# Kernel optimization log

Measured on AMD Instinct MI355X. Metric: run time of the kernel, lower is better.

Reference implementation:

```python
import jax, jax.numpy as jnp
import numpy as np

NB_HEAD = 16
DIM_PER_HEAD = 64
EMB = 1024
B, SQ, SK = 4, 2048, 2048


def setup_inputs() -> dict:
    key = jax.random.key(0)
    ks = jax.random.split(key, 8)
    scale = 1.0 / np.sqrt(EMB)
    return {
        "hidden_state_query": jax.random.normal(ks[0], (B, SQ, EMB), jnp.float32),
        "hidden_state_key": jax.random.normal(ks[1], (B, SK, EMB), jnp.float32),
        "hidden_state_value": jax.random.normal(ks[2], (B, SK, EMB), jnp.float32),
        "attention_mask": jax.random.randint(ks[3], (B, SQ, SK), 0, 2).astype(bool),
        "Wq": jax.random.uniform(ks[4], (NB_HEAD * DIM_PER_HEAD, EMB), jnp.float32, -scale, scale),
        "Wk": jax.random.uniform(ks[5], (NB_HEAD * DIM_PER_HEAD, EMB), jnp.float32, -scale, scale),
        "Wv": jax.random.uniform(ks[6], (NB_HEAD * DIM_PER_HEAD, EMB), jnp.float32, -scale, scale),
        "Wo": jax.random.uniform(ks[7], (EMB, NB_HEAD * DIM_PER_HEAD), jnp.float32, -scale, scale),
    }


def reference(hidden_state_query, hidden_state_key, hidden_state_value,
              attention_mask, Wq, Wk, Wv, Wo):
    bs, sq, _ = hidden_state_query.shape
    sk = hidden_state_key.shape[1]
    # projections (nn.Linear without bias: x @ W.T)
    q = (hidden_state_query @ Wq.T).reshape(bs, sq, NB_HEAD, DIM_PER_HEAD).transpose(0, 2, 1, 3)
    k = (hidden_state_key @ Wk.T).reshape(bs, sk, NB_HEAD, DIM_PER_HEAD).transpose(0, 2, 1, 3)
    v = (hidden_state_value @ Wv.T).reshape(bs, sk, NB_HEAD, DIM_PER_HEAD).transpose(0, 2, 1, 3)
    scores = jnp.einsum('bhqd,bhkd->bhqk', q, k) / jnp.sqrt(jnp.asarray(DIM_PER_HEAD, q.dtype))
    attn = jax.nn.softmax(scores, axis=-1)
    # POST-softmax zero masking (True -> 0), broadcast over heads; no renormalization
    attn = jnp.where(attention_mask[:, None, :, :], jnp.asarray(0.0, attn.dtype), attn)
    ctx = jnp.einsum('bhqk,bhkd->bhqd', attn, v)  # [B,H,Sq,Dh]
    ctx = ctx.transpose(0, 2, 1, 3).reshape(bs, sq, NB_HEAD * DIM_PER_HEAD)
    return ctx @ Wo.T + hidden_state_query
```

## Files before the change

kernel.cpp:

```cpp
#include <hip/hip_runtime.h>
#include <hip/hip_bf16.h>
#include <stdint.h>

typedef __bf16 bf16_t;
typedef bf16_t bf16x2 __attribute__((ext_vector_type(2)));
typedef bf16_t bf16x8 __attribute__((ext_vector_type(8)));
typedef float  f32x4  __attribute__((ext_vector_type(4)));
typedef float  f32x16 __attribute__((ext_vector_type(16)));
typedef unsigned uint2v __attribute__((ext_vector_type(2)));

#define NB_HEAD 16
#define DH      64
#define EMB     1024
#define BATCH   4
#define SEQ     2048
#define NTOK    (BATCH*SEQ)

#define QSCALE 0.1803368801111204f

__device__ __forceinline__ void gload_lds16(const void* g, void* l) {
  __builtin_amdgcn_global_load_lds(
      (const __attribute__((address_space(1))) void*)g,
      (__attribute__((address_space(3))) void*)l, 16, 0, 0);
}

__device__ __forceinline__ uint32_t pkbf(float a, float b) {
  bf16x2 v = { (bf16_t)a, (bf16_t)b };
  return __builtin_bit_cast(uint32_t, v);
}

__device__ __forceinline__ void cvt8_body(const float* __restrict__ in,
                                          bf16_t* __restrict__ out, int i) {
  const float4* p = reinterpret_cast<const float4*>(in) + (size_t)i * 2;
  float4 a = p[0], b = p[1];
  uint4 r;
  r.x = pkbf(a.x, a.y); r.y = pkbf(a.z, a.w);
  r.z = pkbf(b.x, b.y); r.w = pkbf(b.z, b.w);
  reinterpret_cast<uint4*>(out)[i] = r;
}

__device__ __forceinline__ void mkand_body(const uint8_t* __restrict__ m,
                                           uint16_t* __restrict__ out, int i) {
  uint2 v = reinterpret_cast<const uint2*>(m)[i];
  uint4 r;
  uint32_t lo = v.x, hi = v.y;
  uint16_t e[8];
#pragma unroll
  for (int j = 0; j < 4; j++) e[j]     = (uint16_t)(((lo >> (8 * j)) & 0xFF) - 1);
#pragma unroll
  for (int j = 0; j < 4; j++) e[4 + j] = (uint16_t)(((hi >> (8 * j)) & 0xFF) - 1);
  r.x = (uint32_t)e[0] | ((uint32_t)e[1] << 16);
  r.y = (uint32_t)e[2] | ((uint32_t)e[3] << 16);
  r.z = (uint32_t)e[4] | ((uint32_t)e[5] << 16);
  r.w = (uint32_t)e[6] | ((uint32_t)e[7] << 16);
  reinterpret_cast<uint4*>(out)[i] = r;
}

__global__ void __launch_bounds__(256)
prep(const float* __restrict__ hq, const float* __restrict__ hk,
     const float* __restrict__ hv, const float* __restrict__ Wq,
     const float* __restrict__ Wk, const float* __restrict__ Wv,
     const float* __restrict__ Wo,
     bf16_t* hq_b, bf16_t* hk_b, bf16_t* hv_b,
     bf16_t* Wq_b, bf16_t* Wk_b, bf16_t* Wv_b, bf16_t* Wo_b,
     const uint8_t* __restrict__ mask, uint16_t* __restrict__ mand) {
  const int bid = blockIdx.x;
  if (bid < 12288) {
    const int seg = bid >> 12;
    const float* src = seg == 0 ? hq : seg == 1 ? hk : hv;
    bf16_t*      dst = seg == 0 ? hq_b : seg == 1 ? hk_b : hv_b;
    cvt8_body(src, dst, (bid & 4095) * 256 + (int)threadIdx.x);
  } else if (bid < 14336) {
    const int sb = bid - 12288;
    const int seg = sb >> 9;
    const float* src = seg == 0 ? Wq : seg == 1 ? Wk : seg == 2 ? Wv : Wo;
    bf16_t*      dst = seg == 0 ? Wq_b : seg == 1 ? Wk_b : seg == 2 ? Wv_b : Wo_b;
    cvt8_body(src, dst, (sb & 511) * 256 + (int)threadIdx.x);
  } else {
    mkand_body(mask, mand, (bid - 14336) * 256 + (int)threadIdx.x);
  }
}

__global__ void __launch_bounds__(256)
mkand(const uint8_t* __restrict__ m, uint16_t* __restrict__ out) {
  mkand_body(m, out, blockIdx.x * 256 + (int)threadIdx.x);
}

#define BM 128
#define BN 128
#define BKT 32

template<int EPI>
__global__ void __launch_bounds__(256, 4)
gemm_bt(const bf16_t* __restrict__ A, const bf16_t* __restrict__ Bw,
        bf16_t* __restrict__ Cb, float* __restrict__ Cf,
        const float* __restrict__ resid, float qscale) {
  __shared__ bf16_t As[2][BM * BKT];
  __shared__ bf16_t Bs[2][BN * BKT];
  const int K = EMB, N = EMB;
  const int t    = threadIdx.x;
  const int lane = t & 63, w = t >> 6;
  const int wr = w >> 1, wc = w & 1;
  const int l15 = lane & 15, l4 = lane >> 4;

  const int lin = blockIdx.x + 8 * blockIdx.y;
  const int nl  = (lin & 7) * 64 + (lin >> 3);
  const int rowBase = (nl >> 3) * BM, colBase = (nl & 7) * BN;

  f32x4 acc[4][4];
#pragma unroll
  for (int i = 0; i < 4; i++)
#pragma unroll
    for (int j = 0; j < 4; j++) acc[i][j] = f32x4{0.f, 0.f, 0.f, 0.f};

  const int t16 = t * 16;

#pragma unroll
  for (int i = 0; i < 2; ++i) {
    int off  = i * 4096 + t16;
    int row  = off >> 6, colb = off & 63;
    gload_lds16((const char*)A  + (((size_t)(rowBase + row)) * K) * 2 + colb, (char*)As[0] + off);
    gload_lds16((const char*)Bw + (((size_t)(colBase + row)) * K) * 2 + colb, (char*)Bs[0] + off);
  }
  __syncthreads();

  int cur = 0;
  for (int k0 = 0; k0 < K; k0 += BKT) {
    if (k0 + BKT < K) {
      const int nb = cur ^ 1;
#pragma unroll
      for (int i = 0; i < 2; ++i) {
        int off  = i * 4096 + t16;
        int row  = off >> 6, colb = off & 63;
        gload_lds16((const char*)A  + (((size_t)(rowBase + row)) * K + k0 + BKT) * 2 + colb, (char*)As[nb] + off);
        gload_lds16((const char*)Bw + (((size_t)(colBase + row)) * K + k0 + BKT) * 2 + colb, (char*)Bs[nb] + off);
      }
    }
    {
      bf16x8 af[4], bfb[4];
#pragma unroll
      for (int mi = 0; mi < 4; mi++)
        af[mi] = *reinterpret_cast<const bf16x8*>(
            &As[cur][(wr * 64 + mi * 16 + l15) * BKT + l4 * 8]);
#pragma unroll
      for (int ni = 0; ni < 4; ni++)
        bfb[ni] = *reinterpret_cast<const bf16x8*>(
            &Bs[cur][(wc * 64 + ni * 16 + l15) * BKT + l4 * 8]);
      __builtin_amdgcn_s_setprio(1);
#pragma unroll
      for (int mi = 0; mi < 4; mi++)
#pragma unroll
        for (int ni = 0; ni < 4; ni++)
          acc[mi][ni] = __builtin_amdgcn_mfma_f32_16x16x32_bf16(
              af[mi], bfb[ni], acc[mi][ni], 0, 0, 0);
      __builtin_amdgcn_s_setprio(0);
    }
    __syncthreads();
    cur ^= 1;
  }

#pragma unroll
  for (int mi = 0; mi < 4; mi++) {
#pragma unroll
    for (int ni = 0; ni < 4; ni++) {
      const int m0 = rowBase + wr * 64 + mi * 16 + l4 * 4;
      const int n  = colBase + wc * 64 + ni * 16 + l15;
      if (EPI == 1) {
        const int bq = m0 >> 11, s0 = m0 & 2047, hh = n >> 6, d = n & 63;
        size_t local = (size_t)(s0 >> 6) * 4096 + ((s0 >> 4) & 3) * 1024 +
                       (d >> 5) * 512 + ((s0 >> 3) & 1) * 256 + (d & 31) * 8 + (s0 & 7);
        uint2 st;
        st.x = pkbf(acc[mi][ni][0], acc[mi][ni][1]);
        st.y = pkbf(acc[mi][ni][2], acc[mi][ni][3]);
        *reinterpret_cast<uint2*>(Cb + (size_t)(bq * 16 + hh) * 131072 + local) = st;
      } else {
#pragma unroll
        for (int r = 0; r < 4; r++) {
          int m = m0 + r;
          float v = acc[mi][ni][r];
          if (EPI == 0) {
            Cb[(size_t)m * N + n] = (bf16_t)(v * qscale);
          } else if (EPI == 3) {
            const int bq = m >> 11, s = m & 2047, hh = n >> 6, d = n & 63;
            size_t local = (size_t)(s >> 6) * 4096 + ((s >> 5) & 1) * 2048 +
                           (d >> 4) * 512 + ((d >> 3) & 1) * 256 + (s & 31) * 8 + (d & 7);
            Cb[(size_t)(bq * 16 + hh) * 131072 + local] = (bf16_t)v;
          } else {
            Cf[(size_t)m * N + n] = v + resid[(size_t)m * N + n];
          }
        }
      }
    }
  }
}

__global__ void __launch_bounds__(256, 4)
attn32(const bf16_t* __restrict__ Qb, const bf16_t* __restrict__ Kh,
       const bf16_t* __restrict__ Vt, const uint16_t* __restrict__ Mand,
       bf16_t* __restrict__ ctx) {
  __shared__ __align__(16) bf16_t Ks[2][64 * 64];
  __shared__ __align__(16) bf16_t Vs[2][64 * 64];

  const int t = threadIdx.x, lane = t & 63, wid = t >> 6;
  const int q = lane & 31, hi = lane >> 5;
  const int l16 = lane * 16;

  const int lin = blockIdx.x + 16 * (blockIdx.y + 16 * blockIdx.z);
  const int nl  = (lin & 7) * 128 + (lin >> 3);
  const int bx = nl & 15, h = (nl >> 4) & 15, b = nl >> 8;

  const int q0 = bx * 128 + wid * 32;
  const int qrow = b * SEQ + q0 + q;

  const char* kg = (const char*)(Kh + ((size_t)(b * NB_HEAD + h)) * SEQ * DH);
  const char* vg = (const char*)(Vt + ((size_t)(b * NB_HEAD + h)) * SEQ * DH);

  const bf16_t* qp = Qb + (size_t)qrow * EMB + h * DH + hi * 8;
  bf16x8 qf[4];
#pragma unroll
  for (int d = 0; d < 4; d++) qf[d] = *reinterpret_cast<const bf16x8*>(qp + d * 16);

  f32x16 o0 = {0}, o1 = {0};
  float lrun = 0.f;
  const uint16_t* mbase = Mand + (size_t)qrow * SEQ;

  gload_lds16(kg + t * 16,        (char*)Ks[0] + t * 16);
  gload_lds16(kg + 4096 + t * 16, (char*)Ks[0] + 4096 + t * 16);
  gload_lds16(vg + t * 16,        (char*)Vs[0] + t * 16);
  gload_lds16(vg + 4096 + t * 16, (char*)Vs[0] + 4096 + t * 16);
  __syncthreads();

  int cur = 0;
  for (int kb = 0; kb < SEQ; kb += 64) {
    if (kb + 64 < SEQ) {
      const int nb = cur ^ 1;
      const size_t o = (size_t)(kb + 64) * 128;
      gload_lds16(kg + o + t * 16,        (char*)Ks[nb] + t * 16);
      gload_lds16(kg + o + 4096 + t * 16, (char*)Ks[nb] + 4096 + t * 16);
      gload_lds16(vg + o + t * 16,        (char*)Vs[nb] + t * 16);
      gload_lds16(vg + o + 4096 + t * 16, (char*)Vs[nb] + 4096 + t * 16);
    }

    const char* kls = (const char*)Ks[cur];
    f32x16 p0 = {0}, p1 = {0};
    __builtin_amdgcn_s_setprio(1);
#pragma unroll
    for (int dsl = 0; dsl < 4; dsl++) {
      bf16x8 kf0 = *reinterpret_cast<const bf16x8*>(kls + dsl * 1024 + l16);
      bf16x8 kf1 = *reinterpret_cast<const bf16x8*>(kls + 4096 + dsl * 1024 + l16);
      p0 = __builtin_amdgcn_mfma_f32_32x32x16_bf16(kf0, qf[dsl], p0, 0, 0, 0);
      p1 = __builtin_amdgcn_mfma_f32_32x32x16_bf16(kf1, qf[dsl], p1, 0, 0, 0);
    }
    __builtin_amdgcn_s_setprio(0);

    uint4 mv[4];
#pragma unroll
    for (int ks = 0; ks < 4; ks++)
      mv[ks] = *reinterpret_cast<const uint4*>(mbase + kb + 16 * ks + 8 * hi);

    float ps = 0.f;
#pragma unroll
    for (int i = 0; i < 16; i++) { p0[i] = __builtin_amdgcn_exp2f(p0[i]); ps += p0[i]; }
#pragma unroll
    for (int i = 0; i < 16; i++) { p1[i] = __builtin_amdgcn_exp2f(p1[i]); ps += p1[i]; }
    ps += __shfl_xor(ps, 32);
    lrun += ps;

    const char* vls = (const char*)Vs[cur];
#pragma unroll
    for (int ks = 0; ks < 4; ks++) {
      const int s8 = (ks & 1) * 8;
      float e0, e1, e2, e3, e4, e5, e6, e7;
      if (ks < 2) {
        e0 = p0[s8+0]; e1 = p0[s8+1]; e2 = p0[s8+2]; e3 = p0[s8+3];
        e4 = p0[s8+4]; e5 = p0[s8+5]; e6 = p0[s8+6]; e7 = p0[s8+7];
      } else {
        e0 = p1[s8+0]; e1 = p1[s8+1]; e2 = p1[s8+2]; e3 = p1[s8+3];
        e4 = p1[s8+4]; e5 = p1[s8+5]; e6 = p1[s8+6]; e7 = p1[s8+7];
      }
      uint32_t a0 = pkbf(e0, e1), a1 = pkbf(e2, e3);
      uint32_t a2 = pkbf(e4, e5), a3 = pkbf(e6, e7);
      uint2v s02 = __builtin_amdgcn_permlane32_swap(a0, a2, false, false);
      uint2v s13 = __builtin_amdgcn_permlane32_swap(a1, a3, false, false);
      uint4 fr;
      fr.x = s02[0]; fr.y = s13[0]; fr.z = s02[1]; fr.w = s13[1];
      fr.x &= mv[ks].x; fr.y &= mv[ks].y; fr.z &= mv[ks].z; fr.w &= mv[ks].w;
      bf16x8 pa = __builtin_bit_cast(bf16x8, fr);
      bf16x8 vf0 = *reinterpret_cast<const bf16x8*>(vls + ks * 2048 + l16);
      bf16x8 vf1 = *reinterpret_cast<const bf16x8*>(vls + ks * 2048 + 1024 + l16);
      __builtin_amdgcn_s_setprio(1);
      o0 = __builtin_amdgcn_mfma_f32_32x32x16_bf16(vf0, pa, o0, 0, 0, 0);
      o1 = __builtin_amdgcn_mfma_f32_32x32x16_bf16(vf1, pa, o1, 0, 0, 0);
      __builtin_amdgcn_s_setprio(0);
    }

    __syncthreads();
    cur ^= 1;
  }

  float inv = 1.0f / lrun;
  bf16_t* cp = ctx + (size_t)qrow * EMB + h * DH;
#pragma unroll
  for (int g = 0; g < 4; g++) {
    uint2 st;
    st.x = pkbf(o0[4*g+0] * inv, o0[4*g+1] * inv);
    st.y = pkbf(o0[4*g+2] * inv, o0[4*g+3] * inv);
    *reinterpret_cast<uint2*>(cp + 8 * g + 4 * hi) = st;
    st.x = pkbf(o1[4*g+0] * inv, o1[4*g+1] * inv);
    st.y = pkbf(o1[4*g+2] * inv, o1[4*g+3] * inv);
    *reinterpret_cast<uint2*>(cp + 32 + 8 * g + 4 * hi) = st;
  }
}

extern "C" void kernel_launch(void* const* d_in, const int* in_sizes, int n_in,
                              void* d_out, int out_size, void* d_ws, size_t ws_size,
                              hipStream_t stream) {
  const float*   hq   = (const float*)d_in[0];
  const float*   hk   = (const float*)d_in[1];
  const float*   hv   = (const float*)d_in[2];
  const uint8_t* mask = (const uint8_t*)d_in[3];
  const float*   Wq   = (const float*)d_in[4];
  const float*   Wk   = (const float*)d_in[5];
  const float*   Wv   = (const float*)d_in[6];
  const float*   Wo   = (const float*)d_in[7];
  float* out = (float*)d_out;

  char* ws = (char*)d_ws;
  const size_t SZ_H = (size_t)NTOK * EMB * 2;
  const size_t SZ_W = (size_t)EMB * EMB * 2;
  bf16_t* hq_b = (bf16_t*)(ws + 0 * SZ_H);
  bf16_t* hk_b = (bf16_t*)(ws + 1 * SZ_H);
  bf16_t* hv_b = (bf16_t*)(ws + 2 * SZ_H);
  bf16_t* Qb   = (bf16_t*)(ws + 3 * SZ_H);
  bf16_t* Kh   = (bf16_t*)(ws + 4 * SZ_H);
  bf16_t* Vt   = (bf16_t*)(ws + 5 * SZ_H);
  bf16_t* ctx  = (bf16_t*)(ws + 6 * SZ_H);
  bf16_t* Wq_b = (bf16_t*)(ws + 7 * SZ_H + 0 * SZ_W);
  bf16_t* Wk_b = (bf16_t*)(ws + 7 * SZ_H + 1 * SZ_W);
  bf16_t* Wv_b = (bf16_t*)(ws + 7 * SZ_H + 2 * SZ_W);
  bf16_t* Wo_b = (bf16_t*)(ws + 7 * SZ_H + 3 * SZ_W);

  const size_t MAND_OFF = 7 * SZ_H + 4 * SZ_W;
  const size_t MAND_SZ  = (size_t)BATCH * SEQ * SEQ * 2;
  const bool bigws = ws_size >= MAND_OFF + MAND_SZ;
  uint16_t* Mand = bigws ? (uint16_t*)(ws + MAND_OFF) : (uint16_t*)ws;

  prep<<<bigws ? 22528 : 14336, 256, 0, stream>>>(
      hq, hk, hv, Wq, Wk, Wv, Wo,
      hq_b, hk_b, hv_b, Wq_b, Wk_b, Wv_b, Wo_b, mask, Mand);

  dim3 ggrid(EMB / BN, NTOK / BM);
  gemm_bt<0><<<ggrid, 256, 0, stream>>>(hq_b, Wq_b, Qb, nullptr, nullptr, QSCALE);
  gemm_bt<3><<<ggrid, 256, 0, stream>>>(hk_b, Wk_b, Kh, nullptr, nullptr, 1.0f);
  gemm_bt<1><<<ggrid, 256, 0, stream>>>(hv_b, Wv_b, Vt, nullptr, nullptr, 1.0f);

  if (!bigws) mkand<<<8192, 256, 0, stream>>>(mask, Mand);

  attn32<<<dim3(SEQ / 128, NB_HEAD, BATCH), 256, 0, stream>>>(Qb, Kh, Vt, Mand, ctx);

  gemm_bt<2><<<ggrid, 256, 0, stream>>>(ctx, Wo_b, nullptr, out, hq, 1.0f);
}
```

Baseline: 246.0 us.

## Load K/V fragments directly from global memory instead of LDS double buffering

Drops the shared-memory double-buffered K/V staging (global_load_lds plus __syncthreads) in the attention kernel. Each wave now reads its K and V MFMA fragments straight from global memory, relying on L2/L1 to serve the four waves of a block that share the same tile. The s_setprio hints are removed and the loop is kept rolled. This removes LDS traffic and block-wide barriers, but each wave now issues its own redundant global loads with no prefetch, so global load latency sits directly in front of the MFMAs.

```diff
diff --git a/kernel.cpp b/kernel.cpp
--- a/kernel.cpp
+++ b/kernel.cpp
@@ -198,9 +198,6 @@
 attn32(const bf16_t* __restrict__ Qb, const bf16_t* __restrict__ Kh,
        const bf16_t* __restrict__ Vt, const uint16_t* __restrict__ Mand,
        bf16_t* __restrict__ ctx) {
-  __shared__ __align__(16) bf16_t Ks[2][64 * 64];
-  __shared__ __align__(16) bf16_t Vs[2][64 * 64];
-
   const int t = threadIdx.x, lane = t & 63, wid = t >> 6;
   const int q = lane & 31, hi = lane >> 5;
   const int l16 = lane * 16;
@@ -212,8 +209,8 @@
   const int q0 = bx * 128 + wid * 32;
   const int qrow = b * SEQ + q0 + q;
 
-  const char* kg = (const char*)(Kh + ((size_t)(b * NB_HEAD + h)) * SEQ * DH);
-  const char* vg = (const char*)(Vt + ((size_t)(b * NB_HEAD + h)) * SEQ * DH);
+  const char* kg = (const char*)(Kh + ((size_t)(b * NB_HEAD + h)) * SEQ * DH) + l16;
+  const char* vg = (const char*)(Vt + ((size_t)(b * NB_HEAD + h)) * SEQ * DH) + l16;
 
   const bf16_t* qp = Qb + (size_t)qrow * EMB + h * DH + hi * 8;
   bf16x8 qf[4];
@@ -224,34 +221,19 @@
   float lrun = 0.f;
   const uint16_t* mbase = Mand + (size_t)qrow * SEQ;
 
-  gload_lds16(kg + t * 16,        (char*)Ks[0] + t * 16);
-  gload_lds16(kg + 4096 + t * 16, (char*)Ks[0] + 4096 + t * 16);
-  gload_lds16(vg + t * 16,        (char*)Vs[0] + t * 16);
-  gload_lds16(vg + 4096 + t * 16, (char*)Vs[0] + 4096 + t * 16);
-  __syncthreads();
-
-  int cur = 0;
+#pragma unroll 1
   for (int kb = 0; kb < SEQ; kb += 64) {
-    if (kb + 64 < SEQ) {
-      const int nb = cur ^ 1;
-      const size_t o = (size_t)(kb + 64) * 128;
-      gload_lds16(kg + o + t * 16,        (char*)Ks[nb] + t * 16);
-      gload_lds16(kg + o + 4096 + t * 16, (char*)Ks[nb] + 4096 + t * 16);
-      gload_lds16(vg + o + t * 16,        (char*)Vs[nb] + t * 16);
-      gload_lds16(vg + o + 4096 + t * 16, (char*)Vs[nb] + 4096 + t * 16);
-    }
-
-    const char* kls = (const char*)Ks[cur];
+    const char* kgt = kg + (size_t)kb * 128;
+    const char* vgt = vg + (size_t)kb * 128;
+
     f32x16 p0 = {0}, p1 = {0};
-    __builtin_amdgcn_s_setprio(1);
 #pragma unroll
     for (int dsl = 0; dsl < 4; dsl++) {
-      bf16x8 kf0 = *reinterpret_cast<const bf16x8*>(kls + dsl * 1024 + l16);
-      bf16x8 kf1 = *reinterpret_cast<const bf16x8*>(kls + 4096 + dsl * 1024 + l16);
+      bf16x8 kf0 = *reinterpret_cast<const bf16x8*>(kgt + dsl * 1024);
+      bf16x8 kf1 = *reinterpret_cast<const bf16x8*>(kgt + 4096 + dsl * 1024);
       p0 = __builtin_amdgcn_mfma_f32_32x32x16_bf16(kf0, qf[dsl], p0, 0, 0, 0);
       p1 = __builtin_amdgcn_mfma_f32_32x32x16_bf16(kf1, qf[dsl], p1, 0, 0, 0);
     }
-    __builtin_amdgcn_s_setprio(0);
 
     uint4 mv[4];
 #pragma unroll
@@ -266,7 +248,6 @@
     ps += __shfl_xor(ps, 32);
     lrun += ps;
 
-    const char* vls = (const char*)Vs[cur];
 #pragma unroll
     for (int ks = 0; ks < 4; ks++) {
       const int s8 = (ks & 1) * 8;
@@ -286,16 +267,11 @@
       fr.x = s02[0]; fr.y = s13[0]; fr.z = s02[1]; fr.w = s13[1];
       fr.x &= mv[ks].x; fr.y &= mv[ks].y; fr.z &= mv[ks].z; fr.w &= mv[ks].w;
       bf16x8 pa = __builtin_bit_cast(bf16x8, fr);
-      bf16x8 vf0 = *reinterpret_cast<const bf16x8*>(vls + ks * 2048 + l16);
-      bf16x8 vf1 = *reinterpret_cast<const bf16x8*>(vls + ks * 2048 + 1024 + l16);
-      __builtin_amdgcn_s_setprio(1);
+      bf16x8 vf0 = *reinterpret_cast<const bf16x8*>(vgt + ks * 2048);
+      bf16x8 vf1 = *reinterpret_cast<const bf16x8*>(vgt + ks * 2048 + 1024);
       o0 = __builtin_amdgcn_mfma_f32_32x32x16_bf16(vf0, pa, o0, 0, 0, 0);
       o1 = __builtin_amdgcn_mfma_f32_32x32x16_bf16(vf1, pa, o1, 0, 0, 0);
-      __builtin_amdgcn_s_setprio(0);
-    }
-
-    __syncthreads();
-    cur ^= 1;
+    }
   }
 
   float inv = 1.0f / lrun;
```

After: 321.4 us. 30.7% more time.

## Software-pipeline QK^T one tile ahead with triple-buffered K in attention

Applied to the files above, without the earlier changes.

The attention kernel now computes the QK^T scores for the next key tile while the current tile's exp, masking and PV MMAs run. K gets three LDS buffers and V two, rotated by pointer swaps, with a single barrier at the top of each iteration. The aim is to overlap matrix-core work with the softmax and LDS traffic. In exchange it uses more LDS and registers, so launch bounds drop from 4 to 3 waves per SIMD and occupancy falls.

```diff
diff --git a/kernel.cpp b/kernel.cpp
--- a/kernel.cpp
+++ b/kernel.cpp
@@ -194,11 +194,11 @@
   }
 }
 
-__global__ void __launch_bounds__(256, 4)
+__global__ void __launch_bounds__(256, 3)
 attn32(const bf16_t* __restrict__ Qb, const bf16_t* __restrict__ Kh,
        const bf16_t* __restrict__ Vt, const uint16_t* __restrict__ Mand,
        bf16_t* __restrict__ ctx) {
-  __shared__ __align__(16) bf16_t Ks[2][64 * 64];
+  __shared__ __align__(16) bf16_t Ks[3][64 * 64];
   __shared__ __align__(16) bf16_t Vs[2][64 * 64];
 
   const int t = threadIdx.x, lane = t & 63, wid = t >> 6;
@@ -224,39 +224,61 @@
   float lrun = 0.f;
   const uint16_t* mbase = Mand + (size_t)qrow * SEQ;
 
-  gload_lds16(kg + t * 16,        (char*)Ks[0] + t * 16);
-  gload_lds16(kg + 4096 + t * 16, (char*)Ks[0] + 4096 + t * 16);
-  gload_lds16(vg + t * 16,        (char*)Vs[0] + t * 16);
-  gload_lds16(vg + 4096 + t * 16, (char*)Vs[0] + 4096 + t * 16);
+  char* kA = (char*)Ks[0]; char* kB = (char*)Ks[1]; char* kC = (char*)Ks[2];
+  char* vA = (char*)Vs[0]; char* vB = (char*)Vs[1];
+
+  gload_lds16(kg + t * 16,        kA + t * 16);
+  gload_lds16(kg + 4096 + t * 16, kA + 4096 + t * 16);
+  gload_lds16(kg + 8192 + t * 16,        kB + t * 16);
+  gload_lds16(kg + 8192 + 4096 + t * 16, kB + 4096 + t * 16);
+  gload_lds16(vg + t * 16,        vA + t * 16);
+  gload_lds16(vg + 4096 + t * 16, vA + 4096 + t * 16);
   __syncthreads();
 
-  int cur = 0;
-  for (int kb = 0; kb < SEQ; kb += 64) {
-    if (kb + 64 < SEQ) {
-      const int nb = cur ^ 1;
-      const size_t o = (size_t)(kb + 64) * 128;
-      gload_lds16(kg + o + t * 16,        (char*)Ks[nb] + t * 16);
-      gload_lds16(kg + o + 4096 + t * 16, (char*)Ks[nb] + 4096 + t * 16);
-      gload_lds16(vg + o + t * 16,        (char*)Vs[nb] + t * 16);
-      gload_lds16(vg + o + 4096 + t * 16, (char*)Vs[nb] + 4096 + t * 16);
-    }
-
-    const char* kls = (const char*)Ks[cur];
-    f32x16 p0 = {0}, p1 = {0};
-    __builtin_amdgcn_s_setprio(1);
-#pragma unroll
-    for (int dsl = 0; dsl < 4; dsl++) {
-      bf16x8 kf0 = *reinterpret_cast<const bf16x8*>(kls + dsl * 1024 + l16);
-      bf16x8 kf1 = *reinterpret_cast<const bf16x8*>(kls + 4096 + dsl * 1024 + l16);
-      p0 = __builtin_amdgcn_mfma_f32_32x32x16_bf16(kf0, qf[dsl], p0, 0, 0, 0);
-      p1 = __builtin_amdgcn_mfma_f32_32x32x16_bf16(kf1, qf[dsl], p1, 0, 0, 0);
-    }
-    __builtin_amdgcn_s_setprio(0);
+  f32x16 p0 = {0}, p1 = {0};
+  __builtin_amdgcn_s_setprio(1);
+#pragma unroll
+  for (int dsl = 0; dsl < 4; dsl++) {
+    bf16x8 kf0 = *reinterpret_cast<const bf16x8*>(kA + dsl * 1024 + l16);
+    bf16x8 kf1 = *reinterpret_cast<const bf16x8*>(kA + 4096 + dsl * 1024 + l16);
+    p0 = __builtin_amdgcn_mfma_f32_32x32x16_bf16(kf0, qf[dsl], p0, 0, 0, 0);
+    p1 = __builtin_amdgcn_mfma_f32_32x32x16_bf16(kf1, qf[dsl], p1, 0, 0, 0);
+  }
+  __builtin_amdgcn_s_setprio(0);
+
+#pragma unroll 1
+  for (int tt = 0; tt < 32; ++tt) {
+    __syncthreads();
+
+    if (tt + 2 < 32) {
+      const size_t o = (size_t)(tt + 2) * 8192;
+      gload_lds16(kg + o + t * 16,        kC + t * 16);
+      gload_lds16(kg + o + 4096 + t * 16, kC + 4096 + t * 16);
+    }
+    if (tt + 1 < 32) {
+      const size_t o = (size_t)(tt + 1) * 8192;
+      char* vdst = (tt & 1) ? vA : vB;
+      gload_lds16(vg + o + t * 16,        vdst + t * 16);
+      gload_lds16(vg + o + 4096 + t * 16, vdst + 4096 + t * 16);
+    }
+
+    f32x16 n0 = {0}, n1 = {0};
+    if (tt + 1 < 32) {
+      __builtin_amdgcn_s_setprio(1);
+#pragma unroll
+      for (int dsl = 0; dsl < 4; dsl++) {
+        bf16x8 kf0 = *reinterpret_cast<const bf16x8*>(kB + dsl * 1024 + l16);
+        bf16x8 kf1 = *reinterpret_cast<const bf16x8*>(kB + 4096 + dsl * 1024 + l16);
+        n0 = __builtin_amdgcn_mfma_f32_32x32x16_bf16(kf0, qf[dsl], n0, 0, 0, 0);
+        n1 = __builtin_amdgcn_mfma_f32_32x32x16_bf16(kf1, qf[dsl], n1, 0, 0, 0);
+      }
+      __builtin_amdgcn_s_setprio(0);
+    }
 
     uint4 mv[4];
 #pragma unroll
     for (int ks = 0; ks < 4; ks++)
-      mv[ks] = *reinterpret_cast<const uint4*>(mbase + kb + 16 * ks + 8 * hi);
+      mv[ks] = *reinterpret_cast<const uint4*>(mbase + tt * 64 + 16 * ks + 8 * hi);
 
     float ps = 0.f;
 #pragma unroll
@@ -266,7 +288,7 @@
     ps += __shfl_xor(ps, 32);
     lrun += ps;
 
-    const char* vls = (const char*)Vs[cur];
+    const char* vls = (tt & 1) ? vB : vA;
 #pragma unroll
     for (int ks = 0; ks < 4; ks++) {
       const int s8 = (ks & 1) * 8;
@@ -294,8 +316,8 @@
       __builtin_amdgcn_s_setprio(0);
     }
 
-    __syncthreads();
-    cur ^= 1;
+    p0 = n0; p1 = n1;
+    char* ktmp = kA; kA = kB; kB = kC; kC = ktmp;
   }
 
   float inv = 1.0f / lrun;
@@ -332,8 +354,8 @@
   bf16_t* hk_b = (bf16_t*)(ws + 1 * SZ_H);
   bf16_t* hv_b = (bf16_t*)(ws + 2 * SZ_H);
   bf16_t* Qb   = (bf16_t*)(ws + 3 * SZ_H);
-  bf16_t* Kh   = (bf16_t*)(ws + 4 * SZ_H);
-  bf16_t* Vt   = (bf16_t*)(ws + 5 * SZ_H);
+  bf16_t* Kf   = (bf16_t*)(ws + 4 * SZ_H);
+  bf16_t* Vf   = (bf16_t*)(ws + 5 * SZ_H);
   bf16_t* ctx  = (bf16_t*)(ws + 6 * SZ_H);
   bf16_t* Wq_b = (bf16_t*)(ws + 7 * SZ_H + 0 * SZ_W);
   bf16_t* Wk_b = (bf16_t*)(ws + 7 * SZ_H + 1 * SZ_W);
@@ -351,12 +373,12 @@
 
   dim3 ggrid(EMB / BN, NTOK / BM);
   gemm_bt<0><<<ggrid, 256, 0, stream>>>(hq_b, Wq_b, Qb, nullptr, nullptr, QSCALE);
-  gemm_bt<3><<<ggrid, 256, 0, stream>>>(hk_b, Wk_b, Kh, nullptr, nullptr, 1.0f);
-  gemm_bt<1><<<ggrid, 256, 0, stream>>>(hv_b, Wv_b, Vt, nullptr, nullptr, 1.0f);
+  gemm_bt<3><<<ggrid, 256, 0, stream>>>(hk_b, Wk_b, Kf, nullptr, nullptr, 1.0f);
+  gemm_bt<1><<<ggrid, 256, 0, stream>>>(hv_b, Wv_b, Vf, nullptr, nullptr, 1.0f);
 
   if (!bigws) mkand<<<8192, 256, 0, stream>>>(mask, Mand);
 
-  attn32<<<dim3(SEQ / 128, NB_HEAD, BATCH), 256, 0, stream>>>(Qb, Kh, Vt, Mand, ctx);
+  attn32<<<dim3(SEQ / 128, NB_HEAD, BATCH), 256, 0, stream>>>(Qb, Kf, Vf, Mand, ctx);
 
   gemm_bt<2><<<ggrid, 256, 0, stream>>>(ctx, Wo_b, nullptr, out, hq, 1.0f);
 }
```

Result: slower. 260.2 us (+5.8%).
